# Optimization experiments

Measured on AMD Instinct MI355X. Metric: run time of the kernel, lower is better.

## Reference

```python
import jax, jax.numpy as jnp
import numpy as np

EPS = 1e-6

def _rms_norm(t, g):
    # t: [B, S, C] (applied before the view to heads, matching the torch code)
    y = t.astype(jnp.float32)
    y = jax.lax.rsqrt(jnp.mean(y * y, axis=-1, keepdims=True) + EPS)
    return (t * y * g).astype(t.dtype)

def _apply_rope(t, cos, sin):
    # t: [B, S, N, D]; cos/sin: [1, S, 1, D//2]; interleaved pair rotation
    b, s, n, d = t.shape
    tr = t.reshape(b, s, n, d // 2, 2)
    tre, tim = tr[..., 0], tr[..., 1]
    out = jnp.stack([tre * cos - tim * sin, tre * sin + tim * cos], axis=-1)
    return out.reshape(b, s, n, d)

def setup_inputs() -> dict:
    key = jax.random.key(0)
    ks = jax.random.split(key, 8)
    B, S, DIM, N, D = 2, 1024, 3072, 24, 128
    x = jax.random.normal(ks[0], (B, S, DIM), dtype=jnp.float32)
    seq_lens = jax.random.randint(ks[1], (B,), S // 2, S + 1, dtype=jnp.int32)
    grid_sizes = jnp.tile(jnp.array([[16, 8, 8]], dtype=jnp.int32), (B, 1))
    # rope angle table [1024, D//2]: pos * inv_freq
    inv_freq = 1.0 / (10000.0 ** (jnp.arange(D // 2, dtype=jnp.float32) * 2.0 / D))
    freqs = jnp.arange(1024, dtype=jnp.float32)[:, None] * inv_freq[None, :]
    sc = 1.0 / np.sqrt(DIM)
    Wq = jax.random.normal(ks[2], (DIM, DIM), dtype=jnp.float32) * sc
    Wk = jax.random.normal(ks[3], (DIM, DIM), dtype=jnp.float32) * sc
    Wv = jax.random.normal(ks[4], (DIM, DIM), dtype=jnp.float32) * sc
    Wo = jax.random.normal(ks[5], (DIM, DIM), dtype=jnp.float32) * sc
    bq = jnp.zeros((DIM,), jnp.float32); bk = jnp.zeros((DIM,), jnp.float32)
    bv = jnp.zeros((DIM,), jnp.float32); bo = jnp.zeros((DIM,), jnp.float32)
    gq = jnp.ones((DIM,), jnp.float32); gk = jnp.ones((DIM,), jnp.float32)
    return {"x": x, "seq_lens": seq_lens, "grid_sizes": grid_sizes, "freqs": freqs,
            "Wq": Wq, "bq": bq, "Wk": Wk, "bk": bk, "Wv": Wv, "bv": bv,
            "Wo": Wo, "bo": bo, "gq": gq, "gk": gk}

def reference(x, seq_lens, grid_sizes, freqs, Wq, bq, Wk, bk, Wv, bv, Wo, bo, gq, gk):
    b, s, dim = x.shape
    d = 2 * freqs.shape[1]          # head_dim
    n = dim // d                    # num_heads
    q = _rms_norm(x @ Wq.T + bq, gq).reshape(b, s, n, d)
    k = _rms_norm(x @ Wk.T + bk, gk).reshape(b, s, n, d)
    v = (x @ Wv.T + bv).reshape(b, s, n, d)
    ang = freqs[:s]                 # [S, D//2]
    cos = jnp.cos(ang)[None, :, None, :]
    sin = jnp.sin(ang)[None, :, None, :]
    q = _apply_rope(q, cos, sin)
    k = _apply_rope(k, cos, sin)
    # full attention (window_size = (-1,-1)), varlen key masking via seq_lens
    scale = d ** -0.5
    scores = jnp.einsum('bind,bjnd->bnij', q, k) * scale   # [B,N,S,S]
    key_valid = jnp.arange(s)[None, :] < seq_lens[:, None]  # [B,S]
    scores = jnp.where(key_valid[:, None, None, :], scores, jnp.finfo(scores.dtype).min)
    p = jax.nn.softmax(scores, axis=-1)
    out = jnp.einsum('bnij,bjnd->bind', p, v).reshape(b, s, dim)
    return out @ Wo.T + bo
```

## Files before the change

### kernel.cpp

```cpp
#include <hip/hip_runtime.h>
#include <cmath>

#define BB   2
#define SS   1024
#define DIMM 3072
#define NHH  24
#define HDD  128
#define MM   (BB * SS)

typedef _Float16 f16;
typedef __attribute__((ext_vector_type(8))) _Float16 half8;
typedef __attribute__((ext_vector_type(4))) float floatx4;
typedef unsigned int u32;
typedef const __attribute__((address_space(1))) u32* gp1;
typedef __attribute__((address_space(3))) u32* lp3;

__device__ __forceinline__ void gload_lds16(const void* g, void* l) {
    __builtin_amdgcn_global_load_lds((gp1)g, (lp3)l, 16, 0, 0);
}

__global__ __launch_bounds__(256) void cvt_f16_kernel(
    const float* __restrict__ in, f16* __restrict__ outp, int n8)
{
    int i = blockIdx.x * 256 + threadIdx.x;
    if (i >= n8) return;
    const float4* p = (const float4*)(in + (size_t)i * 8);
    float4 a = p[0], b = p[1];
    half8 h = {(f16)a.x, (f16)a.y, (f16)a.z, (f16)a.w,
               (f16)b.x, (f16)b.y, (f16)b.z, (f16)b.w};
    *(half8*)(outp + (size_t)i * 8) = h;
}

template<bool QKV>
__global__ __launch_bounds__(256) void gemm_f16(
    const f16* __restrict__ A,
    const float* __restrict__ W0, const float* __restrict__ W1, const float* __restrict__ W2,
    const float* __restrict__ b0, const float* __restrict__ b1, const float* __restrict__ b2,
    f16* __restrict__ D0, f16* __restrict__ D1, f16* __restrict__ D2,
    float* __restrict__ F)
{
    constexpr int K = DIMM;
    constexpr int NSTEP = K / 32;
    __shared__ f16 As[128 * 32];
    __shared__ f16 Bs[128 * 32];

    const int tid  = threadIdx.x;
    const int lane = tid & 63;
    const int wave = tid >> 6;
    const int wm = wave >> 1, wn = wave & 1;
    const int lr = lane & 15;
    const int lq = lane >> 4;

    const int id  = blockIdx.x;
    const int cpx = (int)gridDim.x >> 3;
    const int swz = (id & 7) * cpx + (id >> 3);
    const int bm = (swz & 15) << 7;
    const int bn = (swz >> 4) << 7;

    const float* W; const float* bias; f16* D = nullptr;
    int nloc = bn;
    if constexpr (QKV) {
        int sel = bn / DIMM;
        nloc = bn - sel * DIMM;
        W    = sel == 0 ? W0 : (sel == 1 ? W1 : W2);
        bias = sel == 0 ? b0 : (sel == 1 ? b1 : b2);
        D    = sel == 0 ? D0 : (sel == 1 ? D1 : D2);
    } else { W = W0; bias = b0; }

    const int r0 = tid >> 2;
    const int c8 = (tid & 3) << 3;
    const float* bp0 = W + (size_t)(nloc + r0) * K + c8;
    const float* bp1 = W + (size_t)(nloc + r0 + 64) * K + c8;

    const int arow_l = lane >> 2;
    const int acol_l = (lane & 3) << 3;
    const f16* agbase = A + (size_t)bm * K;

    float4 sb00, sb01, sb10, sb11;
    auto LOADB = [&](int k0) {
        sb00 = *(const float4*)(bp0 + k0); sb01 = *(const float4*)(bp0 + k0 + 4);
        sb10 = *(const float4*)(bp1 + k0); sb11 = *(const float4*)(bp1 + k0 + 4);
    };
    auto STOREB = [&]() {
        half8 h0 = {(f16)sb00.x, (f16)sb00.y, (f16)sb00.z, (f16)sb00.w,
                    (f16)sb01.x, (f16)sb01.y, (f16)sb01.z, (f16)sb01.w};
        half8 h1 = {(f16)sb10.x, (f16)sb10.y, (f16)sb10.z, (f16)sb10.w,
                    (f16)sb11.x, (f16)sb11.y, (f16)sb11.z, (f16)sb11.w};
        *(half8*)&Bs[r0 * 32 + c8]        = h0;
        *(half8*)&Bs[(r0 + 64) * 32 + c8] = h1;
    };

    floatx4 acc[4][4];
#pragma unroll
    for (int i = 0; i < 4; ++i)
#pragma unroll
        for (int j = 0; j < 4; ++j) acc[i][j] = (floatx4){0.f, 0.f, 0.f, 0.f};

    LOADB(0);
    for (int ks = 0; ks < NSTEP; ++ks) {
        const int k0 = ks * 32;
        __syncthreads();
#pragma unroll
        for (int i = 0; i < 2; ++i) {
            int rbase = wave * 32 + i * 16;
            gload_lds16(agbase + (size_t)(rbase + arow_l) * K + k0 + acol_l,
                        &As[rbase * 32]);
        }
        STOREB();
        __syncthreads();
        if (ks + 1 < NSTEP) LOADB(k0 + 32);

        half8 af[4], bf[4];
#pragma unroll
        for (int i = 0; i < 4; ++i) {
            af[i] = *(const half8*)&As[(wm * 64 + i * 16 + lr) * 32 + lq * 8];
            bf[i] = *(const half8*)&Bs[(wn * 64 + i * 16 + lr) * 32 + lq * 8];
        }
#pragma unroll
        for (int mi = 0; mi < 4; ++mi)
#pragma unroll
            for (int ni = 0; ni < 4; ++ni)
                acc[mi][ni] = __builtin_amdgcn_mfma_f32_16x16x32_f16(af[mi], bf[ni], acc[mi][ni], 0, 0, 0);
    }

    const int crow0 = bm + wm * 64 + (lq << 2);
    const int ccol0 = nloc + wn * 64;
#pragma unroll
    for (int ni = 0; ni < 4; ++ni) {
        const int col = ccol0 + ni * 16 + lr;
        const float bv = bias[col];
#pragma unroll
        for (int mi = 0; mi < 4; ++mi) {
            const int row = crow0 + mi * 16;
#pragma unroll
            for (int r2 = 0; r2 < 4; ++r2) {
                if constexpr (QKV)
                    D[(size_t)(row + r2) * DIMM + col] = (f16)(acc[mi][ni][r2] + bv);
                else
                    F[(size_t)(row + r2) * DIMM + col] = acc[mi][ni][r2] + bv;
            }
        }
    }
}

__global__ __launch_bounds__(192) void rmsnorm_rope_f16(
    f16* __restrict__ q, f16* __restrict__ k,
    const float* __restrict__ gq, const float* __restrict__ gk,
    const float* __restrict__ freqs)
{
    f16* t = (blockIdx.y == 0) ? q : k;
    const float* g = (blockIdx.y == 0) ? gq : gk;
    const int row = blockIdx.x;
    const int s = row & (SS - 1);
    const int tid = threadIdx.x;
    f16* base = t + (size_t)row * DIMM + tid * 16;

    half8 v0 = *(const half8*)base;
    half8 v1 = *(const half8*)(base + 8);
    float v[16];
#pragma unroll
    for (int j = 0; j < 8; ++j) { v[j] = (float)v0[j]; v[8 + j] = (float)v1[j]; }

    float ssq = 0.f;
#pragma unroll
    for (int j = 0; j < 16; ++j) ssq += v[j] * v[j];
#pragma unroll
    for (int off = 32; off > 0; off >>= 1) ssq += __shfl_down(ssq, off, 64);
    __shared__ float red[3];
    if ((tid & 63) == 0) red[tid >> 6] = ssq;
    __syncthreads();
    float tot = red[0] + red[1] + red[2];
    float sc = rsqrtf(tot * (1.0f / (float)DIMM) + 1e-6f);

    const float* gp = g + tid * 16;
    float y[16];
#pragma unroll
    for (int j = 0; j < 16; ++j) y[j] = v[j] * sc * gp[j];

#pragma unroll
    for (int p = 0; p < 8; ++p) {
        int idx = tid * 16 + 2 * p;
        int f = (idx & 127) >> 1;
        float ang = freqs[s * 64 + f];
        float cc = cosf(ang), sn = sinf(ang);
        float e = y[2 * p], o = y[2 * p + 1];
        y[2 * p]     = e * cc - o * sn;
        y[2 * p + 1] = e * sn + o * cc;
    }
    half8 o0, o1;
#pragma unroll
    for (int j = 0; j < 8; ++j) { o0[j] = (f16)y[j]; o1[j] = (f16)y[8 + j]; }
    *(half8*)base       = o0;
    *(half8*)(base + 8) = o1;
}

__global__ __launch_bounds__(256) void flash_attn_f16(
    const f16* __restrict__ Q, const f16* __restrict__ K,
    const f16* __restrict__ V, const int* __restrict__ seq_lens,
    f16* __restrict__ O)
{
    __shared__ f16 QPs[64 * 128];
    __shared__ f16 Ks[64 * 128];
    __shared__ f16 Vt[128 * 64];

    const int tid  = threadIdx.x;
    const int lane = tid & 63;
    const int wave = tid >> 6;
    const int ln = lane & 15;
    const int lq = lane >> 4;
    const int i0 = blockIdx.x * 64;
    const int h  = blockIdx.y;
    const int b  = blockIdx.z;
    const int slen = seq_lens[b];
    const float scale = 0.08838834764831845f;
    const size_t gstride = NHH * HDD;

    const f16* Qg = Q + ((size_t)(b * SS + i0) * NHH + h) * HDD;
#pragma unroll
    for (int rep = 0; rep < 4; ++rep) {
        int u = tid + rep * 256;
        int r = u >> 4, d0 = (u & 15) << 3;
        half8 qv = *(const half8*)(Qg + (size_t)r * gstride + d0);
        *(half8*)(QPs + r * 128 + (d0 ^ ((r & 7) << 3))) = qv;
    }
    __syncthreads();

    half8 qfrag[4];
    {
        int rq = wave * 16 + ln;
#pragma unroll
        for (int ks = 0; ks < 4; ++ks)
            qfrag[ks] = *(const half8*)(QPs + rq * 128 + ((ks * 32 + lq * 8) ^ ((rq & 7) << 3)));
    }

    floatx4 accO[8];
#pragma unroll
    for (int dt = 0; dt < 8; ++dt) accO[dt] = (floatx4){0.f, 0.f, 0.f, 0.f};
    float mrow[4] = {-3.0e38f, -3.0e38f, -3.0e38f, -3.0e38f};
    float lrow[4] = {0.f, 0.f, 0.f, 0.f};

    const int nT = (slen + 63) >> 6;
    for (int t = 0; t < nT; ++t) {
        const int j0g = t * 64;
        __syncthreads();

        const f16* Kg = K + ((size_t)(b * SS + j0g) * NHH + h) * HDD;
#pragma unroll
        for (int rep = 0; rep < 4; ++rep) {
            int u = tid + rep * 256;
            int r = u >> 4, d0 = (u & 15) << 3;
            half8 kv = *(const half8*)(Kg + (size_t)r * gstride + d0);
            *(half8*)(Ks + r * 128 + (d0 ^ ((r & 7) << 3))) = kv;
        }
        const f16* Vg = V + ((size_t)(b * SS + j0g) * NHH + h) * HDD;
#pragma unroll
        for (int rep = 0; rep < 2; ++rep) {
            int u = tid + rep * 256;
            int jp = u & 31, j0 = jp * 2;
            int d0 = (u >> 5) << 3;
            half8 va = *(const half8*)(Vg + (size_t)j0 * gstride + d0);
            half8 vb = *(const half8*)(Vg + (size_t)(j0 + 1) * gstride + d0);
#pragma unroll
            for (int i = 0; i < 8; ++i) {
                int d = d0 + i;
                union { f16 h[2]; u32 w; } pk;
                pk.h[0] = va[i]; pk.h[1] = vb[i];
                *(u32*)(Vt + d * 64 + (j0 ^ ((d & 7) << 3))) = pk.w;
            }
        }
        __syncthreads();

        floatx4 acc_s[4];
#pragma unroll
        for (int nt = 0; nt < 4; ++nt) {
            acc_s[nt] = (floatx4){0.f, 0.f, 0.f, 0.f};
            int rk = nt * 16 + ln;
#pragma unroll
            for (int ks = 0; ks < 4; ++ks) {
                half8 kf = *(const half8*)(Ks + rk * 128 + ((ks * 32 + lq * 8) ^ ((rk & 7) << 3)));
                acc_s[nt] = __builtin_amdgcn_mfma_f32_16x16x32_f16(qfrag[ks], kf, acc_s[nt], 0, 0, 0);
            }
        }

        float s[4][4];
#pragma unroll
        for (int nt = 0; nt < 4; ++nt) {
            int j = j0g + nt * 16 + ln;
            bool valid = (j < slen);
#pragma unroll
            for (int r = 0; r < 4; ++r)
                s[nt][r] = valid ? acc_s[nt][r] * scale : -3.0e38f;
        }
        float fct[4];
#pragma unroll
        for (int r = 0; r < 4; ++r) {
            float m4 = fmaxf(fmaxf(s[0][r], s[1][r]), fmaxf(s[2][r], s[3][r]));
            m4 = fmaxf(m4, __shfl_xor(m4, 1, 64));
            m4 = fmaxf(m4, __shfl_xor(m4, 2, 64));
            m4 = fmaxf(m4, __shfl_xor(m4, 4, 64));
            m4 = fmaxf(m4, __shfl_xor(m4, 8, 64));
            float mn = fmaxf(mrow[r], m4);
            fct[r] = __expf(mrow[r] - mn);
            mrow[r] = mn;
            float ls = 0.f;
#pragma unroll
            for (int nt = 0; nt < 4; ++nt) {
                float p = __expf(s[nt][r] - mn);
                s[nt][r] = p;
                ls += p;
            }
            ls += __shfl_xor(ls, 1, 64);
            ls += __shfl_xor(ls, 2, 64);
            ls += __shfl_xor(ls, 4, 64);
            ls += __shfl_xor(ls, 8, 64);
            lrow[r] = lrow[r] * fct[r] + ls;
        }

#pragma unroll
        for (int nt = 0; nt < 4; ++nt) {
#pragma unroll
            for (int r = 0; r < 4; ++r) {
                int rw = lq * 4 + r;
                int j = nt * 16 + ln;
                QPs[(wave * 16 + rw) * 128 + (j ^ ((rw & 7) << 3))] = (f16)s[nt][r];
            }
        }

#pragma unroll
        for (int dt = 0; dt < 8; ++dt)
#pragma unroll
            for (int r = 0; r < 4; ++r) accO[dt][r] *= fct[r];

        half8 pfrag[2];
#pragma unroll
        for (int js = 0; js < 2; ++js)
            pfrag[js] = *(const half8*)(QPs + (wave * 16 + ln) * 128 + ((js * 32 + lq * 8) ^ ((ln & 7) << 3)));
#pragma unroll
        for (int dt = 0; dt < 8; ++dt) {
            int d = dt * 16 + ln;
#pragma unroll
            for (int js = 0; js < 2; ++js) {
                half8 vf = *(const half8*)(Vt + d * 64 + ((js * 32 + lq * 8) ^ ((d & 7) << 3)));
                accO[dt] = __builtin_amdgcn_mfma_f32_16x16x32_f16(pfrag[js], vf, accO[dt], 0, 0, 0);
            }
        }
    }

    float linv[4];
#pragma unroll
    for (int r = 0; r < 4; ++r) linv[r] = 1.0f / lrow[r];
    f16* Og = O + ((size_t)(b * SS + i0) * NHH + h) * HDD;
#pragma unroll
    for (int dt = 0; dt < 8; ++dt) {
#pragma unroll
        for (int r = 0; r < 4; ++r) {
            int qr = wave * 16 + lq * 4 + r;
            int d = dt * 16 + ln;
            Og[(size_t)qr * gstride + d] = (f16)(accO[dt][r] * linv[r]);
        }
    }
}

extern "C" void kernel_launch(void* const* d_in, const int* in_sizes, int n_in,
                              void* d_out, int out_size, void* d_ws, size_t ws_size,
                              hipStream_t stream)
{
    const float* x     = (const float*)d_in[0];
    const int*   seq   = (const int*)d_in[1];
    const float* freqs = (const float*)d_in[3];
    const float* Wq    = (const float*)d_in[4];
    const float* bq    = (const float*)d_in[5];
    const float* Wk    = (const float*)d_in[6];
    const float* bk    = (const float*)d_in[7];
    const float* Wv    = (const float*)d_in[8];
    const float* bv    = (const float*)d_in[9];
    const float* Wo    = (const float*)d_in[10];
    const float* bo    = (const float*)d_in[11];
    const float* gq    = (const float*)d_in[12];
    const float* gk    = (const float*)d_in[13];

    float* out = (float*)d_out;
    const size_t MD = (size_t)MM * DIMM;

    f16* X16 = (f16*)d_ws;
    f16* q16 = X16 + MD;
    f16* k16 = X16 + 2 * MD;
    f16* v16 = (f16*)d_out;

    cvt_f16_kernel<<<(int)(MD / (256 * 8)), 256, 0, stream>>>(x, X16, (int)(MD / 8));
    gemm_f16<true><<<(MM / 128) * (3 * DIMM / 128), 256, 0, stream>>>(
        X16, Wq, Wk, Wv, bq, bk, bv, q16, k16, v16, nullptr);
    rmsnorm_rope_f16<<<dim3(MM, 2), 192, 0, stream>>>(q16, k16, gq, gk, freqs);
    flash_attn_f16<<<dim3(SS / 64, NHH, BB), 256, 0, stream>>>(q16, k16, v16, seq, X16);
    gemm_f16<false><<<(MM / 128) * (DIMM / 128), 256, 0, stream>>>(
        X16, Wo, nullptr, nullptr, bo, nullptr, nullptr, nullptr, nullptr, nullptr, out);
}
```

Baseline: 386.7 us.

## Double-buffer GEMM LDS tiles with XOR swizzle to overlap loads and MFMA

The GEMM main loop moves to two LDS buffers for A and B. The next k-tile's async global-to-LDS load of A and the register load of B are issued before the MFMAs on the current tile, and B is stored after them. This leaves one barrier per iteration instead of two. An XOR swizzle on the 16-byte column chunk is applied to both the LDS writes and the fragment reads to cut bank conflicts, and launch bounds now request 3 blocks per CU. LDS use doubles and the register budget is tighter, which could limit occupancy or cause spills.

```diff
diff --git a/kernel.cpp b/kernel.cpp
--- a/kernel.cpp
+++ b/kernel.cpp
@@ -32,7 +32,7 @@
 }
 
 template<bool QKV>
-__global__ __launch_bounds__(256) void gemm_f16(
+__global__ __launch_bounds__(256, 3) void gemm_f16(
     const f16* __restrict__ A,
     const float* __restrict__ W0, const float* __restrict__ W1, const float* __restrict__ W2,
     const float* __restrict__ b0, const float* __restrict__ b1, const float* __restrict__ b2,
@@ -41,8 +41,8 @@
 {
     constexpr int K = DIMM;
     constexpr int NSTEP = K / 32;
-    __shared__ f16 As[128 * 32];
-    __shared__ f16 Bs[128 * 32];
+    __shared__ f16 As[2][128 * 32];
+    __shared__ f16 Bs[2][128 * 32];
 
     const int tid  = threadIdx.x;
     const int lane = tid & 63;
@@ -69,11 +69,12 @@
 
     const int r0 = tid >> 2;
     const int c8 = (tid & 3) << 3;
+    const int c8sw = c8 ^ ((r0 & 3) << 3);
     const float* bp0 = W + (size_t)(nloc + r0) * K + c8;
     const float* bp1 = W + (size_t)(nloc + r0 + 64) * K + c8;
 
     const int arow_l = lane >> 2;
-    const int acol_l = (lane & 3) << 3;
+    const int acol_sw = (((lane & 3) ^ (arow_l & 3)) << 3);
     const f16* agbase = A + (size_t)bm * K;
 
     float4 sb00, sb01, sb10, sb11;
@@ -81,46 +82,58 @@
         sb00 = *(const float4*)(bp0 + k0); sb01 = *(const float4*)(bp0 + k0 + 4);
         sb10 = *(const float4*)(bp1 + k0); sb11 = *(const float4*)(bp1 + k0 + 4);
     };
-    auto STOREB = [&]() {
+    auto STOREB = [&](int buf) {
         half8 h0 = {(f16)sb00.x, (f16)sb00.y, (f16)sb00.z, (f16)sb00.w,
                     (f16)sb01.x, (f16)sb01.y, (f16)sb01.z, (f16)sb01.w};
         half8 h1 = {(f16)sb10.x, (f16)sb10.y, (f16)sb10.z, (f16)sb10.w,
                     (f16)sb11.x, (f16)sb11.y, (f16)sb11.z, (f16)sb11.w};
-        *(half8*)&Bs[r0 * 32 + c8]        = h0;
-        *(half8*)&Bs[(r0 + 64) * 32 + c8] = h1;
+        *(half8*)&Bs[buf][r0 * 32 + c8sw]        = h0;
+        *(half8*)&Bs[buf][(r0 + 64) * 32 + c8sw] = h1;
     };
-
-    floatx4 acc[4][4];
-#pragma unroll
-    for (int i = 0; i < 4; ++i)
-#pragma unroll
-        for (int j = 0; j < 4; ++j) acc[i][j] = (floatx4){0.f, 0.f, 0.f, 0.f};
-
-    LOADB(0);
-    for (int ks = 0; ks < NSTEP; ++ks) {
-        const int k0 = ks * 32;
-        __syncthreads();
+    auto STAGEA = [&](int k0, int buf) {
 #pragma unroll
         for (int i = 0; i < 2; ++i) {
             int rbase = wave * 32 + i * 16;
-            gload_lds16(agbase + (size_t)(rbase + arow_l) * K + k0 + acol_l,
-                        &As[rbase * 32]);
-        }
-        STOREB();
-        __syncthreads();
-        if (ks + 1 < NSTEP) LOADB(k0 + 32);
+            gload_lds16(agbase + (size_t)(rbase + arow_l) * K + k0 + acol_sw,
+                        &As[buf][rbase * 32]);
+        }
+    };
+
+    floatx4 acc[4][4];
+#pragma unroll
+    for (int i = 0; i < 4; ++i)
+#pragma unroll
+        for (int j = 0; j < 4; ++j) acc[i][j] = (floatx4){0.f, 0.f, 0.f, 0.f};
+
+    STAGEA(0, 0);
+    LOADB(0);
+    STOREB(0);
+    __syncthreads();
+
+    for (int ks = 0; ks < NSTEP; ++ks) {
+        const int cur = ks & 1, nxt = cur ^ 1;
+        const bool more = (ks + 1 < NSTEP);
+        if (more) {
+            STAGEA((ks + 1) * 32, nxt);
+            LOADB((ks + 1) * 32);
+        }
 
         half8 af[4], bf[4];
 #pragma unroll
         for (int i = 0; i < 4; ++i) {
-            af[i] = *(const half8*)&As[(wm * 64 + i * 16 + lr) * 32 + lq * 8];
-            bf[i] = *(const half8*)&Bs[(wn * 64 + i * 16 + lr) * 32 + lq * 8];
+            int ra = wm * 64 + i * 16 + lr;
+            int rb = wn * 64 + i * 16 + lr;
+            af[i] = *(const half8*)&As[cur][ra * 32 + ((lq << 3) ^ ((ra & 3) << 3))];
+            bf[i] = *(const half8*)&Bs[cur][rb * 32 + ((lq << 3) ^ ((rb & 3) << 3))];
         }
 #pragma unroll
         for (int mi = 0; mi < 4; ++mi)
 #pragma unroll
             for (int ni = 0; ni < 4; ++ni)
                 acc[mi][ni] = __builtin_amdgcn_mfma_f32_16x16x32_f16(af[mi], bf[ni], acc[mi][ni], 0, 0, 0);
+
+        if (more) STOREB(nxt);
+        __syncthreads();
     }
 
     const int crow0 = bm + wm * 64 + (lq << 2);
```

Result: slower. 419.3 us (+8.4%).

## Multi-buffer GEMM LDS tiles with manual waitcnt pipelining and MFMA priority

Applied to the files above, without the earlier changes.

Rewrites the GEMM main loop to use a four-deep ring of A tiles staged directly to LDS and double-buffered B tiles. The loop issues global loads for future k-steps while computing the current one, with explicit s_waitcnt and s_barrier in place of a pair of __syncthreads per step. It also raises wave priority around the MFMA block. The aim is to hide global-load latency and cut barrier stalls, at the cost of more LDS use and fragile hand-counted vmcnt values that could race if they are wrong.

```diff
diff --git a/kernel.cpp b/kernel.cpp
--- a/kernel.cpp
+++ b/kernel.cpp
@@ -41,8 +41,9 @@
 {
     constexpr int K = DIMM;
     constexpr int NSTEP = K / 32;
-    __shared__ f16 As[128 * 32];
-    __shared__ f16 Bs[128 * 32];
+    constexpr int TS = 128 * 32;
+    __shared__ __align__(16) f16 As[4 * TS];
+    __shared__ __align__(16) f16 Bs[2 * TS];
 
     const int tid  = threadIdx.x;
     const int lane = tid & 63;
@@ -76,51 +77,75 @@
     const int acol_l = (lane & 3) << 3;
     const f16* agbase = A + (size_t)bm * K;
 
-    float4 sb00, sb01, sb10, sb11;
-    auto LOADB = [&](int k0) {
-        sb00 = *(const float4*)(bp0 + k0); sb01 = *(const float4*)(bp0 + k0 + 4);
-        sb10 = *(const float4*)(bp1 + k0); sb11 = *(const float4*)(bp1 + k0 + 4);
+    float4 sA[4], sB[4];
+    auto LOADB = [&](int t, float4* s) {
+        const int k0 = t * 32;
+        s[0] = *(const float4*)(bp0 + k0); s[1] = *(const float4*)(bp0 + k0 + 4);
+        s[2] = *(const float4*)(bp1 + k0); s[3] = *(const float4*)(bp1 + k0 + 4);
     };
-    auto STOREB = [&]() {
-        half8 h0 = {(f16)sb00.x, (f16)sb00.y, (f16)sb00.z, (f16)sb00.w,
-                    (f16)sb01.x, (f16)sb01.y, (f16)sb01.z, (f16)sb01.w};
-        half8 h1 = {(f16)sb10.x, (f16)sb10.y, (f16)sb10.z, (f16)sb10.w,
-                    (f16)sb11.x, (f16)sb11.y, (f16)sb11.z, (f16)sb11.w};
-        *(half8*)&Bs[r0 * 32 + c8]        = h0;
-        *(half8*)&Bs[(r0 + 64) * 32 + c8] = h1;
+    auto STOREB = [&](f16* Bbuf, const float4* s) {
+        half8 h0 = {(f16)s[0].x, (f16)s[0].y, (f16)s[0].z, (f16)s[0].w,
+                    (f16)s[1].x, (f16)s[1].y, (f16)s[1].z, (f16)s[1].w};
+        half8 h1 = {(f16)s[2].x, (f16)s[2].y, (f16)s[2].z, (f16)s[2].w,
+                    (f16)s[3].x, (f16)s[3].y, (f16)s[3].z, (f16)s[3].w};
+        *(half8*)&Bbuf[r0 * 32 + c8]        = h0;
+        *(half8*)&Bbuf[(r0 + 64) * 32 + c8] = h1;
     };
-
-    floatx4 acc[4][4];
-#pragma unroll
-    for (int i = 0; i < 4; ++i)
-#pragma unroll
-        for (int j = 0; j < 4; ++j) acc[i][j] = (floatx4){0.f, 0.f, 0.f, 0.f};
-
-    LOADB(0);
-    for (int ks = 0; ks < NSTEP; ++ks) {
-        const int k0 = ks * 32;
-        __syncthreads();
+    auto STAGEA = [&](int t, int buf) {
+        const int k0 = t * 32;
 #pragma unroll
         for (int i = 0; i < 2; ++i) {
             int rbase = wave * 32 + i * 16;
             gload_lds16(agbase + (size_t)(rbase + arow_l) * K + k0 + acol_l,
-                        &As[rbase * 32]);
-        }
-        STOREB();
-        __syncthreads();
-        if (ks + 1 < NSTEP) LOADB(k0 + 32);
-
+                        &As[buf * TS + rbase * 32]);
+        }
+    };
+
+    floatx4 acc[4][4];
+#pragma unroll
+    for (int i = 0; i < 4; ++i)
+#pragma unroll
+        for (int j = 0; j < 4; ++j) acc[i][j] = (floatx4){0.f, 0.f, 0.f, 0.f};
+
+    auto COMPUTE = [&](const f16* Ac, const f16* Bc) {
         half8 af[4], bf[4];
 #pragma unroll
         for (int i = 0; i < 4; ++i) {
-            af[i] = *(const half8*)&As[(wm * 64 + i * 16 + lr) * 32 + lq * 8];
-            bf[i] = *(const half8*)&Bs[(wn * 64 + i * 16 + lr) * 32 + lq * 8];
-        }
+            af[i] = *(const half8*)&Ac[(wm * 64 + i * 16 + lr) * 32 + lq * 8];
+            bf[i] = *(const half8*)&Bc[(wn * 64 + i * 16 + lr) * 32 + lq * 8];
+        }
+        __builtin_amdgcn_s_setprio(1);
 #pragma unroll
         for (int mi = 0; mi < 4; ++mi)
 #pragma unroll
             for (int ni = 0; ni < 4; ++ni)
                 acc[mi][ni] = __builtin_amdgcn_mfma_f32_16x16x32_f16(af[mi], bf[ni], acc[mi][ni], 0, 0, 0);
+        __builtin_amdgcn_s_setprio(0);
+    };
+
+    LOADB(0, sA);
+    STAGEA(0, 0);
+    LOADB(1, sB);
+    STAGEA(1, 1);
+    STOREB(&Bs[0], sA);
+    asm volatile("s_waitcnt vmcnt(6)" ::: "memory");
+    asm volatile("s_waitcnt lgkmcnt(0)" ::: "memory");
+    __builtin_amdgcn_s_barrier();
+
+    for (int ks = 0; ks < NSTEP; ks += 2) {
+        if (ks + 2 < NSTEP) { LOADB(ks + 2, sA); STAGEA(ks + 2, (ks + 2) & 3); }
+        asm volatile("s_waitcnt vmcnt(12)" ::: "memory");
+        __builtin_amdgcn_s_barrier();
+        STOREB(&Bs[TS], sB);
+        COMPUTE(&As[(ks & 3) * TS], &Bs[0]);
+        asm volatile("s_waitcnt lgkmcnt(0)" ::: "memory");
+
+        if (ks + 3 < NSTEP) { LOADB(ks + 3, sB); STAGEA(ks + 3, (ks + 3) & 3); }
+        asm volatile("s_waitcnt vmcnt(12)" ::: "memory");
+        __builtin_amdgcn_s_barrier();
+        if (ks + 2 < NSTEP) STOREB(&Bs[0], sA);
+        COMPUTE(&As[((ks + 1) & 3) * TS], &Bs[TS]);
+        asm volatile("s_waitcnt lgkmcnt(0)" ::: "memory");
     }
 
     const int crow0 = bm + wm * 64 + (lq << 2);
@@ -199,9 +224,9 @@
     const f16* __restrict__ V, const int* __restrict__ seq_lens,
     f16* __restrict__ O)
 {
-    __shared__ f16 QPs[64 * 128];
-    __shared__ f16 Ks[64 * 128];
-    __shared__ f16 Vt[128 * 64];
+    __shared__ __align__(16) f16 QPs[64 * 128];
+    __shared__ __align__(16) f16 Ks[64 * 128];
+    __shared__ __align__(16) f16 Vt[128 * 64];
 
     const int tid  = threadIdx.x;
     const int lane = tid & 63;
```

After: 353.7 us. 8.5% less time.

## Load fp32 weights directly to LDS with swizzle, convert on fragment read

Applied to the files above, without the earlier changes.

The GEMM now stages the fp32 weight tile straight into shared memory with global_load_lds, instead of loading it into registers, converting to f16 and storing it. Conversion to f16 happens when each wave reads its B fragments. Both the A and B tiles use XOR-swizzled layouts to avoid LDS bank conflicts, and the MFMA block runs at raised wave priority. In exchange, the register-prefetch overlap of the next B tile is gone because loads are now waited on with vmcnt(0) each step, LDS use for B doubles, and every wave repeats the conversion work.

```diff
diff --git a/kernel.cpp b/kernel.cpp
--- a/kernel.cpp
+++ b/kernel.cpp
@@ -41,8 +41,8 @@
 {
     constexpr int K = DIMM;
     constexpr int NSTEP = K / 32;
-    __shared__ f16 As[128 * 32];
-    __shared__ f16 Bs[128 * 32];
+    __shared__ __align__(16) f16   As[128 * 32];
+    __shared__ __align__(16) float Bw[128 * 32];
 
     const int tid  = threadIdx.x;
     const int lane = tid & 63;
@@ -67,28 +67,13 @@
         D    = sel == 0 ? D0 : (sel == 1 ? D1 : D2);
     } else { W = W0; bias = b0; }
 
-    const int r0 = tid >> 2;
-    const int c8 = (tid & 3) << 3;
-    const float* bp0 = W + (size_t)(nloc + r0) * K + c8;
-    const float* bp1 = W + (size_t)(nloc + r0 + 64) * K + c8;
-
-    const int arow_l = lane >> 2;
-    const int acol_l = (lane & 3) << 3;
-    const f16* agbase = A + (size_t)bm * K;
-
-    float4 sb00, sb01, sb10, sb11;
-    auto LOADB = [&](int k0) {
-        sb00 = *(const float4*)(bp0 + k0); sb01 = *(const float4*)(bp0 + k0 + 4);
-        sb10 = *(const float4*)(bp1 + k0); sb11 = *(const float4*)(bp1 + k0 + 4);
-    };
-    auto STOREB = [&]() {
-        half8 h0 = {(f16)sb00.x, (f16)sb00.y, (f16)sb00.z, (f16)sb00.w,
-                    (f16)sb01.x, (f16)sb01.y, (f16)sb01.z, (f16)sb01.w};
-        half8 h1 = {(f16)sb10.x, (f16)sb10.y, (f16)sb10.z, (f16)sb10.w,
-                    (f16)sb11.x, (f16)sb11.y, (f16)sb11.z, (f16)sb11.w};
-        *(half8*)&Bs[r0 * 32 + c8]        = h0;
-        *(half8*)&Bs[(r0 + 64) * 32 + c8] = h1;
-    };
+    const int arow = (lane >> 2);
+    const int acol = ((lane & 3) ^ ((lane >> 3) & 3)) << 3;
+    const f16* agbase = A + (size_t)(bm + arow) * K + acol;
+
+    const int brow = (lane >> 3);
+    const int bcol = ((lane & 7) ^ (lane >> 3)) << 2;
+    const float* wgbase = W + (size_t)(nloc + brow) * K + bcol;
 
     floatx4 acc[4][4];
 #pragma unroll
@@ -96,31 +81,49 @@
 #pragma unroll
         for (int j = 0; j < 4; ++j) acc[i][j] = (floatx4){0.f, 0.f, 0.f, 0.f};
 
-    LOADB(0);
+    const int aswz = ((lr >> 1) & 3) << 3;
+    const int bswz = (lr & 7) << 2;
+
     for (int ks = 0; ks < NSTEP; ++ks) {
         const int k0 = ks * 32;
         __syncthreads();
 #pragma unroll
         for (int i = 0; i < 2; ++i) {
             int rbase = wave * 32 + i * 16;
-            gload_lds16(agbase + (size_t)(rbase + arow_l) * K + k0 + acol_l,
-                        &As[rbase * 32]);
-        }
-        STOREB();
+            gload_lds16(agbase + (size_t)rbase * K + k0, &As[rbase * 32]);
+        }
+#pragma unroll
+        for (int i = 0; i < 4; ++i) {
+            int rbase = wave * 32 + i * 8;
+            gload_lds16(wgbase + (size_t)rbase * K + k0, &Bw[rbase * 32]);
+        }
+        asm volatile("s_waitcnt vmcnt(0)" ::: "memory");
         __syncthreads();
-        if (ks + 1 < NSTEP) LOADB(k0 + 32);
 
         half8 af[4], bf[4];
 #pragma unroll
         for (int i = 0; i < 4; ++i) {
-            af[i] = *(const half8*)&As[(wm * 64 + i * 16 + lr) * 32 + lq * 8];
-            bf[i] = *(const half8*)&Bs[(wn * 64 + i * 16 + lr) * 32 + lq * 8];
-        }
+            int ra = wm * 64 + i * 16 + lr;
+            af[i] = *(const half8*)&As[ra * 32 + ((lq << 3) ^ aswz)];
+        }
+#pragma unroll
+        for (int i = 0; i < 4; ++i) {
+            int rb = wn * 64 + i * 16 + lr;
+            const float* bp = &Bw[rb * 32];
+            int e0 = ((lq << 3) ^ bswz);
+            int e1 = (((lq << 3) + 4) ^ bswz);
+            float4 v0 = *(const float4*)(bp + e0);
+            float4 v1 = *(const float4*)(bp + e1);
+            bf[i] = (half8){(f16)v0.x, (f16)v0.y, (f16)v0.z, (f16)v0.w,
+                            (f16)v1.x, (f16)v1.y, (f16)v1.z, (f16)v1.w};
+        }
+        __builtin_amdgcn_s_setprio(1);
 #pragma unroll
         for (int mi = 0; mi < 4; ++mi)
 #pragma unroll
             for (int ni = 0; ni < 4; ++ni)
                 acc[mi][ni] = __builtin_amdgcn_mfma_f32_16x16x32_f16(af[mi], bf[ni], acc[mi][ni], 0, 0, 0);
+        __builtin_amdgcn_s_setprio(0);
     }
 
     const int crow0 = bm + wm * 64 + (lq << 2);
@@ -199,9 +202,9 @@
     const f16* __restrict__ V, const int* __restrict__ seq_lens,
     f16* __restrict__ O)
 {
-    __shared__ f16 QPs[64 * 128];
-    __shared__ f16 Ks[64 * 128];
-    __shared__ f16 Vt[128 * 64];
+    __shared__ __align__(16) f16 QPs[64 * 128];
+    __shared__ __align__(16) f16 Ks[64 * 128];
+    __shared__ __align__(16) f16 Vt[128 * 64];
 
     const int tid  = threadIdx.x;
     const int lane = tid & 63;
```

Measured after the change: 380.9 us. Within noise of the previous version (-1.5%).
